# Kernel optimization log

Hardware: AMD Instinct MI355X
Metric: run time of the kernel (lower is better)

The kernel has to match this reference:

```python
import jax, jax.numpy as jnp
import numpy as np

N_NODES = 100000
N_EDGES = 1600000
N_GRAPHS = 2000
N_FEAT = 128
HIDDEN = 128
N_LAYERS = 4
BN_EPS = 1e-5


def setup_inputs() -> dict:
    key = jax.random.key(0)
    ks = jax.random.split(key, 8)
    x = jax.random.normal(ks[0], (N_NODES, N_FEAT), dtype=jnp.float32)
    edge_index = jax.random.randint(ks[1], (2, N_EDGES), 0, N_NODES, dtype=jnp.int32)
    batch = jnp.sort(jax.random.randint(ks[2], (N_NODES,), 0, N_GRAPHS, dtype=jnp.int32))
    # layer weights scaled down to keep activations stable over 4 layers
    Ws = jax.random.normal(ks[3], (N_LAYERS, HIDDEN, HIDDEN), dtype=jnp.float32) * 0.1
    bs = jnp.zeros((N_LAYERS, HIDDEN), jnp.float32)
    gammas = jnp.ones((N_LAYERS, HIDDEN), jnp.float32)
    betas = jnp.zeros((N_LAYERS, HIDDEN), jnp.float32)
    run_mean = jnp.zeros((N_LAYERS, HIDDEN), jnp.float32)
    run_var = jnp.ones((N_LAYERS, HIDDEN), jnp.float32)
    W_out = jax.random.normal(ks[4], (HIDDEN, 5), dtype=jnp.float32) * 0.1
    b_out = jnp.zeros((5,), jnp.float32)
    return {"x": x, "edge_index": edge_index, "batch": batch, "Ws": Ws, "bs": bs,
            "gammas": gammas, "betas": betas, "run_mean": run_mean, "run_var": run_var,
            "W_out": W_out, "b_out": b_out}


def _gcn_conv(x, src, dst, norm, self_coef, W, b):
    xw = x @ W                                        # [N, H]
    coef = norm[src] * norm[dst]                      # [E]
    msgs = xw[src] * coef[:, None]                    # [E, H] gather
    agg = jax.ops.segment_sum(msgs, dst, num_segments=N_NODES)  # scatter-add
    agg = agg + xw * self_coef[:, None]               # self-loop term
    return agg + b


def reference(x, edge_index, batch, Ws, bs, gammas, betas, run_mean, run_var, W_out, b_out):
    src, dst = edge_index[0], edge_index[1]
    # degree (incl. self-loop) from destination index
    deg = jax.ops.segment_sum(jnp.ones((N_EDGES,), x.dtype), dst, num_segments=N_NODES) + 1.0
    norm = jax.lax.rsqrt(deg)
    self_coef = norm * norm
    h = x
    for l in range(N_LAYERS):
        h = _gcn_conv(h, src, dst, norm, self_coef, Ws[l], bs[l])
        # BatchNorm1d in eval mode (running stats); dropout is identity in eval
        h = (h - run_mean[l]) * (gammas[l] * jax.lax.rsqrt(run_var[l] + BN_EPS)) + betas[l]
        h = jax.nn.relu(h)
    # global mean pool over graphs
    sums = jax.ops.segment_sum(h, batch, num_segments=N_GRAPHS)
    counts = jax.ops.segment_sum(jnp.ones((N_NODES,), h.dtype), batch, num_segments=N_GRAPHS)
    pooled = sums / jnp.maximum(counts, 1.0)[:, None]  # [G, H]
    return pooled @ W_out + b_out                      # [G, 5]
```

## Files before the change

kernel.cpp:

```cpp
#include <hip/hip_runtime.h>
#include <hip/hip_fp16.h>

#define N_NODES_C 100000
#define N_EDGES_C 1600000
#define N_GRAPHS_C 2000
#define HID 128
#define BN_EPS_C 1e-5f
#define NBUCK 391
#define PART_TILE 4096

typedef _Float16 half8 __attribute__((ext_vector_type(8)));
typedef float float4v __attribute__((ext_vector_type(4)));


__global__ __launch_bounds__(256) void kb_hist(const int* __restrict__ dst, int* __restrict__ bcount) {
    __shared__ int hist[NBUCK];
    const int t = threadIdx.x;
    for (int b = t; b < NBUCK; b += 256) hist[b] = 0;
    __syncthreads();
    const int e0 = blockIdx.x * PART_TILE;
    #pragma unroll
    for (int k = 0; k < 16; k++) {
        int e = e0 + k * 256 + t;
        if (e < N_EDGES_C) atomicAdd(&hist[dst[e] >> 8], 1);
    }
    __syncthreads();
    for (int b = t; b < NBUCK; b += 256) {
        int c = hist[b];
        if (c) atomicAdd(&bcount[b], c);
    }
}

__global__ __launch_bounds__(512) void kb_scan(const int* __restrict__ bcount,
                                               int* __restrict__ bbase, int* __restrict__ bcursor) {
    __shared__ int s[512];
    const int t = threadIdx.x;
    int v = (t < NBUCK) ? bcount[t] : 0;
    s[t] = v;
    __syncthreads();
    for (int off = 1; off < 512; off <<= 1) {
        int u = (t >= off) ? s[t - off] : 0;
        __syncthreads();
        s[t] += u;
        __syncthreads();
    }
    if (t < NBUCK) { int e = s[t] - v; bbase[t] = e; bcursor[t] = e; }
    if (t == 0) bbase[NBUCK] = N_EDGES_C;
}

__global__ __launch_bounds__(256) void kb_part(const int* __restrict__ src, const int* __restrict__ dst,
                                               int* __restrict__ bcursor, int* __restrict__ ebuf) {
    __shared__ int hist[NBUCK];
    __shared__ int startA[NBUCK];
    __shared__ int lcur[NBUCK];
    const int t = threadIdx.x;
    for (int b = t; b < NBUCK; b += 256) { hist[b] = 0; lcur[b] = 0; }
    __syncthreads();
    const int e0 = blockIdx.x * PART_TILE;
    #pragma unroll
    for (int k = 0; k < 16; k++) {
        int e = e0 + k * 256 + t;
        if (e < N_EDGES_C) atomicAdd(&hist[dst[e] >> 8], 1);
    }
    __syncthreads();
    for (int b = t; b < NBUCK; b += 256) {
        int c = hist[b];
        startA[b] = c ? atomicAdd(&bcursor[b], c) : 0;
    }
    __syncthreads();
    #pragma unroll
    for (int k = 0; k < 16; k++) {
        int e = e0 + k * 256 + t;
        if (e < N_EDGES_C) {
            int d = dst[e];
            int b = d >> 8;
            int pos = startA[b] + atomicAdd(&lcur[b], 1);
            ebuf[pos] = (src[e] << 8) | (d & 255);
        }
    }
}

__global__ __launch_bounds__(256) void kb_fill(const int* __restrict__ ebuf, const int* __restrict__ bbase,
                                               int* __restrict__ csr_src, int* __restrict__ offs,
                                               float* __restrict__ norm) {
    __shared__ int s[256];
    __shared__ int excl[256];
    __shared__ int lcur[256];
    const int b = blockIdx.x, t = threadIdx.x;
    const int base = b << 8;
    const int e0 = bbase[b], e1 = bbase[b + 1];
    s[t] = 0; lcur[t] = 0;
    __syncthreads();
    for (int e = e0 + t; e < e1; e += 256)
        atomicAdd(&s[ebuf[e] & 255], 1);
    __syncthreads();
    int own = s[t];
    for (int off = 1; off < 256; off <<= 1) {
        int v = (t >= off) ? s[t - off] : 0;
        __syncthreads();
        s[t] += v;
        __syncthreads();
    }
    excl[t] = s[t] - own;
    int node = base + t;
    if (node < N_NODES_C) {
        offs[node] = e0 + (s[t] - own);
        norm[node] = rsqrtf((float)own + 1.0f);
    }
    if (b == 0 && t == 0) offs[N_NODES_C] = N_EDGES_C;
    __syncthreads();
    for (int e = e0 + t; e < e1; e += 256) {
        int p = ebuf[e];
        int l = p & 255;
        int pos = e0 + excl[l] + atomicAdd(&lcur[l], 1);
        csr_src[pos] = p >> 8;
    }
}


__global__ __launch_bounds__(256) void k_tw(const float* __restrict__ Ws_all, _Float16* __restrict__ WT) {
    int idx = blockIdx.x * 256 + threadIdx.x;
    int l = idx >> 14, r = idx & 16383, k = r >> 7, n = r & 127;
    WT[l * 16384 + n * HID + k] = (_Float16)Ws_all[idx];
}


template<bool F32A>
__global__ __launch_bounds__(256) void k_gemm(const void* __restrict__ Ap,
                                              const _Float16* __restrict__ WT,
                                              const float* __restrict__ norm,
                                              _Float16* __restrict__ Y, int nrows) {
    __shared__ _Float16 Wt[HID][136];
    const int tid = threadIdx.x;
    #pragma unroll
    for (int t = 0; t < 8; t++) {
        int off = tid * 8 + t * 2048;
        half8 v = *(const half8*)&WT[off];
        *(half8*)&Wt[off >> 7][off & 127] = v;
    }
    __syncthreads();

    const int wave = tid >> 6, lane = tid & 63, quad = lane >> 4, l16 = lane & 15;
    half8 Wf[2][4];
    #pragma unroll
    for (int c = 0; c < 2; c++)
        #pragma unroll
        for (int ks = 0; ks < 4; ks++)
            Wf[c][ks] = *(const half8*)&Wt[(wave * 2 + c) * 16 + l16][ks * 32 + quad * 8];

    const int nbase = blockIdx.x * 128;
    #pragma unroll
    for (int t = 0; t < 8; t++) {
        int node = nbase + t * 16 + l16;
        bool ok = node < nrows;
        half8 Af[4];
        if (F32A) {
            const float* arow = (const float*)Ap + (long)node * HID;
            #pragma unroll
            for (int ks = 0; ks < 4; ks++) {
                if (ok) {
                    float4 fa = *(const float4*)&arow[ks * 32 + quad * 8];
                    float4 fb = *(const float4*)&arow[ks * 32 + quad * 8 + 4];
                    _Float16 pk[8] = {(_Float16)fa.x, (_Float16)fa.y, (_Float16)fa.z, (_Float16)fa.w,
                                      (_Float16)fb.x, (_Float16)fb.y, (_Float16)fb.z, (_Float16)fb.w};
                    Af[ks] = *(half8*)pk;
                } else Af[ks] = half8{};
            }
        } else {
            const _Float16* arow = (const _Float16*)Ap + (long)node * HID;
            #pragma unroll
            for (int ks = 0; ks < 4; ks++)
                Af[ks] = ok ? *(const half8*)&arow[ks * 32 + quad * 8] : half8{};
        }
        float4v a0 = {0.f, 0.f, 0.f, 0.f}, a1 = {0.f, 0.f, 0.f, 0.f};
        #pragma unroll
        for (int ks = 0; ks < 4; ks++) {
            a0 = __builtin_amdgcn_mfma_f32_16x16x32_f16(Wf[0][ks], Af[ks], a0, 0, 0, 0);
            a1 = __builtin_amdgcn_mfma_f32_16x16x32_f16(Wf[1][ks], Af[ks], a1, 0, 0, 0);
        }
        float nv = ok ? norm[node] : 0.f;
        _Float16 p0[4], p1[4];
        #pragma unroll
        for (int r = 0; r < 4; r++) {
            p0[r] = (_Float16)(a0[r] * nv);
            p1[r] = (_Float16)(a1[r] * nv);
        }
        *(ushort4*)&Y[(long)node * HID + (wave * 2 + 0) * 16 + quad * 4] = *(ushort4*)p0;
        *(ushort4*)&Y[(long)node * HID + (wave * 2 + 1) * 16 + quad * 4] = *(ushort4*)p1;
    }
}


__global__ __launch_bounds__(256) void k_agg(const __half* __restrict__ y, const int* __restrict__ offs,
                                             const int* __restrict__ csr_src, const float* __restrict__ norm,
                                             const float* __restrict__ bias, const float* __restrict__ mean,
                                             const float* __restrict__ gamma, const float* __restrict__ var,
                                             const float* __restrict__ beta, __half* __restrict__ h) {
    const int wave = __builtin_amdgcn_readfirstlane(threadIdx.x >> 6);
    const int lane = threadIdx.x & 63;
    const int i = blockIdx.x * 4 + wave;
    const int j = lane * 2;

    float2 f = __half22float2(*(const __half2*)&y[(long)i * HID + j]);
    float acc0 = f.x, acc1 = f.y;

    const int e0 = offs[i], e1 = offs[i + 1];
    int e = e0;
    do {
        int id[16];
        #pragma unroll
        for (int u = 0; u < 16; u++) {
            int raw = csr_src[e + u];
            id[u] = (e + u < e1) ? raw : N_NODES_C;
        }
        #pragma unroll
        for (int u = 0; u < 16; u++) {
            float2 g = __half22float2(*(const __half2*)&y[(long)id[u] * HID + j]);
            acc0 += g.x; acc1 += g.y;
        }
        e += 16;
    } while (e < e1);

    const float ni = norm[i];
    float2 bi = *(const float2*)&bias[j];
    float2 me = *(const float2*)&mean[j];
    float2 ga = *(const float2*)&gamma[j];
    float2 va = *(const float2*)&var[j];
    float2 be = *(const float2*)&beta[j];
    float v0 = (acc0 * ni + bi.x - me.x) * (ga.x * rsqrtf(va.x + BN_EPS_C)) + be.x;
    float v1 = (acc1 * ni + bi.y - me.y) * (ga.y * rsqrtf(va.y + BN_EPS_C)) + be.y;
    *(__half2*)&h[(long)i * HID + j] = __floats2half2_rn(fmaxf(v0, 0.f), fmaxf(v1, 0.f));
}


__global__ __launch_bounds__(128) void k_pool(const __half* __restrict__ h, const int* __restrict__ batch,
                                              float* __restrict__ psum, int* __restrict__ pcount) {
    const int j = threadIdx.x;
    const int i0 = blockIdx.x * 32;
    const int iend = min(i0 + 32, N_NODES_C);
    if (i0 >= N_NODES_C) return;
    float acc = 0.f;
    int cur = batch[i0];
    int runStart = i0;
    for (int i = i0; i < iend; i++) {
        int g = batch[i];
        if (g != cur) {
            atomicAdd(&psum[(long)cur * HID + j], acc);
            if (j == 0) atomicAdd(&pcount[cur], i - runStart);
            acc = 0.f; cur = g; runStart = i;
        }
        acc += __half2float(h[(long)i * HID + j]);
    }
    atomicAdd(&psum[(long)cur * HID + j], acc);
    if (j == 0) atomicAdd(&pcount[cur], iend - runStart);
}

__global__ __launch_bounds__(128) void k_final(const float* __restrict__ psum, const int* __restrict__ pcount,
                                               const float* __restrict__ W_out, const float* __restrict__ b_out,
                                               float* __restrict__ out) {
    __shared__ float red[128][5];
    const int g = blockIdx.x, j = threadIdx.x;
    float cnt = fmaxf((float)pcount[g], 1.f);
    float p = psum[(long)g * HID + j] / cnt;
    #pragma unroll
    for (int o = 0; o < 5; o++) red[j][o] = p * W_out[j * 5 + o];
    __syncthreads();
    for (int off = 64; off >= 1; off >>= 1) {
        if (j < off) {
            #pragma unroll
            for (int o = 0; o < 5; o++) red[j][o] += red[j + off][o];
        }
        __syncthreads();
    }
    if (j < 5) out[g * 5 + j] = red[0][j] + b_out[j];
}


extern "C" void kernel_launch(void* const* d_in, const int* in_sizes, int n_in,
                              void* d_out, int out_size, void* d_ws, size_t ws_size,
                              hipStream_t stream) {
    const float* x        = (const float*)d_in[0];
    const int*   eidx     = (const int*)d_in[1];
    const int*   src      = eidx;
    const int*   dst      = eidx + N_EDGES_C;
    const int*   batch    = (const int*)d_in[2];
    const float* Ws_all   = (const float*)d_in[3];
    const float* bs       = (const float*)d_in[4];
    const float* gammas   = (const float*)d_in[5];
    const float* betas    = (const float*)d_in[6];
    const float* run_mean = (const float*)d_in[7];
    const float* run_var  = (const float*)d_in[8];
    const float* W_out    = (const float*)d_in[9];
    const float* b_out    = (const float*)d_in[10];
    float* out = (float*)d_out;

    char* wp = (char*)d_ws;
    auto alloc = [&](size_t bytes) { char* p = wp; wp += (bytes + 255) & ~(size_t)255; return p; };
    __half*   h       = (__half*)alloc((size_t)N_NODES_C * HID * 2);
    _Float16* y       = (_Float16*)alloc((size_t)(N_NODES_C + 128) * HID * 2);
    int*      ebuf    = (int*)y;
    _Float16* WT      = (_Float16*)alloc((size_t)4 * HID * HID * 2);
    int*      csr_src = (int*)alloc((size_t)(N_EDGES_C + 16) * 4);
    int*      offs    = (int*)alloc((size_t)(N_NODES_C + 1) * 4);
    float*    norm    = (float*)alloc((size_t)N_NODES_C * 4);
    int*      bbase   = (int*)alloc((NBUCK + 1) * 4);
    int*      bcursor = (int*)alloc((NBUCK + 1) * 4);
    char*     zbeg    = wp;
    float*    psum    = (float*)alloc((size_t)N_GRAPHS_C * HID * 4);
    int*      pcount  = (int*)alloc((size_t)N_GRAPHS_C * 4);
    int*      bcount  = (int*)alloc((NBUCK + 1) * 4);
    size_t    zlen    = (size_t)(wp - zbeg);

    hipMemsetAsync(zbeg, 0, zlen, stream);

    k_tw<<<256, 256, 0, stream>>>(Ws_all, WT);

    const int PB = (N_EDGES_C + PART_TILE - 1) / PART_TILE;
    kb_hist<<<PB, 256, 0, stream>>>(dst, bcount);
    kb_scan<<<1, 512, 0, stream>>>(bcount, bbase, bcursor);
    kb_part<<<PB, 256, 0, stream>>>(src, dst, bcursor, ebuf);
    kb_fill<<<NBUCK, 256, 0, stream>>>(ebuf, bbase, csr_src, offs, norm);

    const int GB = (N_NODES_C + 127) / 128;
    const int AB = (N_NODES_C + 3) / 4;
    for (int l = 0; l < 4; l++) {
        const void* A = (l == 0) ? (const void*)x : (const void*)h;
        if (l == 0)
            k_gemm<true><<<GB, 256, 0, stream>>>(A, WT, norm, y, N_NODES_C);
        else
            k_gemm<false><<<GB, 256, 0, stream>>>(A, WT + (size_t)l * HID * HID, norm, y, N_NODES_C);
        k_agg<<<AB, 256, 0, stream>>>((const __half*)y, offs, csr_src, norm,
                                      bs + l * HID, run_mean + l * HID, gammas + l * HID,
                                      run_var + l * HID, betas + l * HID, (__half*)h);
    }
    const int PB2 = (N_NODES_C + 31) / 32;
    k_pool <<<PB2, 128, 0, stream>>>((const __half*)h, batch, psum, pcount);
    k_final<<<N_GRAPHS_C, 128, 0, stream>>>(psum, pcount, W_out, b_out, out);
}
```

Measured before the change: 502.0 us.

## Fuse all stages into one persistent cooperative kernel with grid syncs

Replaces the chain of separate launches (memset, weight transpose, CSR build, per-layer GEMM and aggregation, pooling, final projection) with a single cooperative persistent kernel. The stages are separated by grid.sync and use grid-stride loops over the old block indices. The intent is to remove per-launch overhead and inter-kernel gaps. In exchange it adds grid-wide barrier costs and limits the kernel to a fixed resident grid sized from occupancy, which may cut latency hiding in the gather-heavy aggregation phase.

Result: slower. 1.607 ms (+220.1%).

```diff
diff --git a/kernel.cpp b/kernel.cpp
--- a/kernel.cpp
+++ b/kernel.cpp
@@ -1,5 +1,8 @@
 #include <hip/hip_runtime.h>
 #include <hip/hip_fp16.h>
+#include <hip/hip_cooperative_groups.h>
+
+namespace cg = cooperative_groups;
 
 #define N_NODES_C 100000
 #define N_EDGES_C 1600000
@@ -8,271 +11,312 @@
 #define BN_EPS_C 1e-5f
 #define NBUCK 391
 #define PART_TILE 4096
+#define PB_C 391
+#define GB_C 782
+#define AB_C 25000
+#define PU_C 3125
 
 typedef _Float16 half8 __attribute__((ext_vector_type(8)));
 typedef float float4v __attribute__((ext_vector_type(4)));
 
-
-__global__ __launch_bounds__(256) void kb_hist(const int* __restrict__ dst, int* __restrict__ bcount) {
-    __shared__ int hist[NBUCK];
-    const int t = threadIdx.x;
-    for (int b = t; b < NBUCK; b += 256) hist[b] = 0;
-    __syncthreads();
-    const int e0 = blockIdx.x * PART_TILE;
-    #pragma unroll
-    for (int k = 0; k < 16; k++) {
-        int e = e0 + k * 256 + t;
-        if (e < N_EDGES_C) atomicAdd(&hist[dst[e] >> 8], 1);
-    }
-    __syncthreads();
-    for (int b = t; b < NBUCK; b += 256) {
-        int c = hist[b];
-        if (c) atomicAdd(&bcount[b], c);
-    }
-}
-
-__global__ __launch_bounds__(512) void kb_scan(const int* __restrict__ bcount,
-                                               int* __restrict__ bbase, int* __restrict__ bcursor) {
-    __shared__ int s[512];
-    const int t = threadIdx.x;
-    int v = (t < NBUCK) ? bcount[t] : 0;
-    s[t] = v;
-    __syncthreads();
-    for (int off = 1; off < 512; off <<= 1) {
-        int u = (t >= off) ? s[t - off] : 0;
-        __syncthreads();
-        s[t] += u;
-        __syncthreads();
-    }
-    if (t < NBUCK) { int e = s[t] - v; bbase[t] = e; bcursor[t] = e; }
-    if (t == 0) bbase[NBUCK] = N_EDGES_C;
-}
-
-__global__ __launch_bounds__(256) void kb_part(const int* __restrict__ src, const int* __restrict__ dst,
-                                               int* __restrict__ bcursor, int* __restrict__ ebuf) {
-    __shared__ int hist[NBUCK];
-    __shared__ int startA[NBUCK];
-    __shared__ int lcur[NBUCK];
-    const int t = threadIdx.x;
-    for (int b = t; b < NBUCK; b += 256) { hist[b] = 0; lcur[b] = 0; }
-    __syncthreads();
-    const int e0 = blockIdx.x * PART_TILE;
-    #pragma unroll
-    for (int k = 0; k < 16; k++) {
-        int e = e0 + k * 256 + t;
-        if (e < N_EDGES_C) atomicAdd(&hist[dst[e] >> 8], 1);
-    }
-    __syncthreads();
-    for (int b = t; b < NBUCK; b += 256) {
-        int c = hist[b];
-        startA[b] = c ? atomicAdd(&bcursor[b], c) : 0;
-    }
-    __syncthreads();
-    #pragma unroll
-    for (int k = 0; k < 16; k++) {
-        int e = e0 + k * 256 + t;
-        if (e < N_EDGES_C) {
-            int d = dst[e];
-            int b = d >> 8;
-            int pos = startA[b] + atomicAdd(&lcur[b], 1);
-            ebuf[pos] = (src[e] << 8) | (d & 255);
-        }
-    }
-}
-
-__global__ __launch_bounds__(256) void kb_fill(const int* __restrict__ ebuf, const int* __restrict__ bbase,
-                                               int* __restrict__ csr_src, int* __restrict__ offs,
-                                               float* __restrict__ norm) {
-    __shared__ int s[256];
-    __shared__ int excl[256];
-    __shared__ int lcur[256];
-    const int b = blockIdx.x, t = threadIdx.x;
-    const int base = b << 8;
-    const int e0 = bbase[b], e1 = bbase[b + 1];
-    s[t] = 0; lcur[t] = 0;
-    __syncthreads();
-    for (int e = e0 + t; e < e1; e += 256)
-        atomicAdd(&s[ebuf[e] & 255], 1);
-    __syncthreads();
-    int own = s[t];
-    for (int off = 1; off < 256; off <<= 1) {
-        int v = (t >= off) ? s[t - off] : 0;
-        __syncthreads();
-        s[t] += v;
-        __syncthreads();
-    }
-    excl[t] = s[t] - own;
-    int node = base + t;
-    if (node < N_NODES_C) {
-        offs[node] = e0 + (s[t] - own);
-        norm[node] = rsqrtf((float)own + 1.0f);
-    }
-    if (b == 0 && t == 0) offs[N_NODES_C] = N_EDGES_C;
-    __syncthreads();
-    for (int e = e0 + t; e < e1; e += 256) {
-        int p = ebuf[e];
-        int l = p & 255;
-        int pos = e0 + excl[l] + atomicAdd(&lcur[l], 1);
-        csr_src[pos] = p >> 8;
-    }
-}
-
-
-__global__ __launch_bounds__(256) void k_tw(const float* __restrict__ Ws_all, _Float16* __restrict__ WT) {
-    int idx = blockIdx.x * 256 + threadIdx.x;
-    int l = idx >> 14, r = idx & 16383, k = r >> 7, n = r & 127;
-    WT[l * 16384 + n * HID + k] = (_Float16)Ws_all[idx];
-}
-
-
-template<bool F32A>
-__global__ __launch_bounds__(256) void k_gemm(const void* __restrict__ Ap,
-                                              const _Float16* __restrict__ WT,
-                                              const float* __restrict__ norm,
-                                              _Float16* __restrict__ Y, int nrows) {
-    __shared__ _Float16 Wt[HID][136];
-    const int tid = threadIdx.x;
-    #pragma unroll
-    for (int t = 0; t < 8; t++) {
-        int off = tid * 8 + t * 2048;
-        half8 v = *(const half8*)&WT[off];
-        *(half8*)&Wt[off >> 7][off & 127] = v;
-    }
-    __syncthreads();
-
-    const int wave = tid >> 6, lane = tid & 63, quad = lane >> 4, l16 = lane & 15;
-    half8 Wf[2][4];
-    #pragma unroll
-    for (int c = 0; c < 2; c++)
-        #pragma unroll
-        for (int ks = 0; ks < 4; ks++)
-            Wf[c][ks] = *(const half8*)&Wt[(wave * 2 + c) * 16 + l16][ks * 32 + quad * 8];
-
-    const int nbase = blockIdx.x * 128;
-    #pragma unroll
-    for (int t = 0; t < 8; t++) {
-        int node = nbase + t * 16 + l16;
-        bool ok = node < nrows;
-        half8 Af[4];
-        if (F32A) {
-            const float* arow = (const float*)Ap + (long)node * HID;
-            #pragma unroll
-            for (int ks = 0; ks < 4; ks++) {
-                if (ok) {
-                    float4 fa = *(const float4*)&arow[ks * 32 + quad * 8];
-                    float4 fb = *(const float4*)&arow[ks * 32 + quad * 8 + 4];
-                    _Float16 pk[8] = {(_Float16)fa.x, (_Float16)fa.y, (_Float16)fa.z, (_Float16)fa.w,
-                                      (_Float16)fb.x, (_Float16)fb.y, (_Float16)fb.z, (_Float16)fb.w};
-                    Af[ks] = *(half8*)pk;
-                } else Af[ks] = half8{};
+constexpr size_t al(size_t v) { return (v + 255) & ~(size_t)255; }
+constexpr size_t OFF_H    = 0;
+constexpr size_t OFF_Y    = al(OFF_H    + (size_t)N_NODES_C * HID * 2);
+constexpr size_t OFF_WT   = al(OFF_Y    + (size_t)(N_NODES_C + 128) * HID * 2);
+constexpr size_t OFF_CSR  = al(OFF_WT   + (size_t)4 * HID * HID * 2);
+constexpr size_t OFF_OFFS = al(OFF_CSR  + (size_t)(N_EDGES_C + 16) * 4);
+constexpr size_t OFF_NORM = al(OFF_OFFS + (size_t)(N_NODES_C + 1) * 4);
+constexpr size_t OFF_BB   = al(OFF_NORM + (size_t)N_NODES_C * 4);
+constexpr size_t OFF_BCUR = al(OFF_BB   + (NBUCK + 1) * 4);
+constexpr size_t OFF_ZERO = al(OFF_BCUR + (NBUCK + 1) * 4);
+constexpr size_t OFF_PSUM = OFF_ZERO;
+constexpr size_t OFF_PCNT = al(OFF_PSUM + (size_t)N_GRAPHS_C * HID * 4);
+constexpr size_t OFF_BCNT = al(OFF_PCNT + (size_t)N_GRAPHS_C * 4);
+constexpr size_t OFF_END  = al(OFF_BCNT + (NBUCK + 1) * 4);
+
+union SM {
+    _Float16 Wt[HID][136];
+    struct { int hist[NBUCK], startA[NBUCK], lcur[NBUCK]; } part;
+    struct { int s[256], excl[256], lcur[256]; } fill;
+    int scan[512];
+    float red[2][128][5];
+};
+
+__global__ __launch_bounds__(256, 4) void k_mega(
+    const float* __restrict__ x, const int* __restrict__ eidx, const int* __restrict__ batch,
+    const float* __restrict__ Ws_all, const float* __restrict__ bs, const float* __restrict__ gammas,
+    const float* __restrict__ betas, const float* __restrict__ run_mean, const float* __restrict__ run_var,
+    const float* __restrict__ W_out, const float* __restrict__ b_out, float* __restrict__ out,
+    char* __restrict__ ws)
+{
+    __shared__ SM sm;
+    cg::grid_group grid = cg::this_grid();
+    const int tid = threadIdx.x, bid = blockIdx.x, G = gridDim.x;
+    const int* src = eidx;
+    const int* dst = eidx + N_EDGES_C;
+
+    __half*   h      = (__half*)(ws + OFF_H);
+    _Float16* y      = (_Float16*)(ws + OFF_Y);
+    int*      ebuf   = (int*)(ws + OFF_Y);
+    _Float16* WT     = (_Float16*)(ws + OFF_WT);
+    int*      csr    = (int*)(ws + OFF_CSR);
+    int*      offs   = (int*)(ws + OFF_OFFS);
+    float*    norm   = (float*)(ws + OFF_NORM);
+    int*      bbase  = (int*)(ws + OFF_BB);
+    int*      bcur   = (int*)(ws + OFF_BCUR);
+    float*    psum   = (float*)(ws + OFF_PSUM);
+    int*      pcount = (int*)(ws + OFF_PCNT);
+    int*      bcount = (int*)(ws + OFF_BCNT);
+
+    {
+        int* zp = (int*)(ws + OFF_ZERO);
+        const int zn = (int)((OFF_END - OFF_ZERO) >> 2);
+        for (int i = bid * 256 + tid; i < zn; i += G * 256) zp[i] = 0;
+        for (int i = bid * 256 + tid; i < 4 * HID * HID; i += G * 256) {
+            int l = i >> 14, r = i & 16383, k = r >> 7, n = r & 127;
+            WT[l * 16384 + n * HID + k] = (_Float16)Ws_all[i];
+        }
+    }
+    grid.sync();
+
+    for (int c = bid; c < PB_C; c += G) {
+        for (int b = tid; b < NBUCK; b += 256) sm.part.hist[b] = 0;
+        __syncthreads();
+        const int e0 = c * PART_TILE;
+        #pragma unroll
+        for (int k = 0; k < 16; k++) {
+            int e = e0 + k * 256 + tid;
+            if (e < N_EDGES_C) atomicAdd(&sm.part.hist[dst[e] >> 8], 1);
+        }
+        __syncthreads();
+        for (int b = tid; b < NBUCK; b += 256) {
+            int cc = sm.part.hist[b];
+            if (cc) atomicAdd(&bcount[b], cc);
+        }
+        __syncthreads();
+    }
+    grid.sync();
+
+    if (bid == 0) {
+        int v0 = (tid < NBUCK) ? bcount[tid] : 0;
+        int v1 = (tid + 256 < NBUCK) ? bcount[tid + 256] : 0;
+        sm.scan[tid] = v0; sm.scan[tid + 256] = v1;
+        __syncthreads();
+        for (int off = 1; off < 512; off <<= 1) {
+            int a = (tid >= off) ? sm.scan[tid - off] : 0;
+            int b = (tid + 256 >= off) ? sm.scan[tid + 256 - off] : 0;
+            __syncthreads();
+            sm.scan[tid] += a; sm.scan[tid + 256] += b;
+            __syncthreads();
+        }
+        if (tid < NBUCK) { int e = sm.scan[tid] - v0; bbase[tid] = e; bcur[tid] = e; }
+        if (tid + 256 < NBUCK) { int e = sm.scan[tid + 256] - v1; bbase[tid + 256] = e; bcur[tid + 256] = e; }
+        if (tid == 0) bbase[NBUCK] = N_EDGES_C;
+    }
+    grid.sync();
+
+    for (int c = bid; c < PB_C; c += G) {
+        for (int b = tid; b < NBUCK; b += 256) { sm.part.hist[b] = 0; sm.part.lcur[b] = 0; }
+        __syncthreads();
+        const int e0 = c * PART_TILE;
+        #pragma unroll
+        for (int k = 0; k < 16; k++) {
+            int e = e0 + k * 256 + tid;
+            if (e < N_EDGES_C) atomicAdd(&sm.part.hist[dst[e] >> 8], 1);
+        }
+        __syncthreads();
+        for (int b = tid; b < NBUCK; b += 256) {
+            int cc = sm.part.hist[b];
+            sm.part.startA[b] = cc ? atomicAdd(&bcur[b], cc) : 0;
+        }
+        __syncthreads();
+        #pragma unroll
+        for (int k = 0; k < 16; k++) {
+            int e = e0 + k * 256 + tid;
+            if (e < N_EDGES_C) {
+                int d = dst[e];
+                int b = d >> 8;
+                int pos = sm.part.startA[b] + atomicAdd(&sm.part.lcur[b], 1);
+                ebuf[pos] = (src[e] << 8) | (d & 255);
             }
-        } else {
-            const _Float16* arow = (const _Float16*)Ap + (long)node * HID;
+        }
+        __syncthreads();
+    }
+    grid.sync();
+
+    for (int b = bid; b < NBUCK; b += G) {
+        const int base = b << 8;
+        const int e0 = bbase[b], e1 = bbase[b + 1];
+        sm.fill.s[tid] = 0; sm.fill.lcur[tid] = 0;
+        __syncthreads();
+        for (int e = e0 + tid; e < e1; e += 256)
+            atomicAdd(&sm.fill.s[ebuf[e] & 255], 1);
+        __syncthreads();
+        int own = sm.fill.s[tid];
+        for (int off = 1; off < 256; off <<= 1) {
+            int v = (tid >= off) ? sm.fill.s[tid - off] : 0;
+            __syncthreads();
+            sm.fill.s[tid] += v;
+            __syncthreads();
+        }
+        sm.fill.excl[tid] = sm.fill.s[tid] - own;
+        int node = base + tid;
+        if (node < N_NODES_C) {
+            offs[node] = e0 + sm.fill.excl[tid];
+            norm[node] = rsqrtf((float)own + 1.0f);
+        }
+        if (b == 0 && tid == 0) offs[N_NODES_C] = N_EDGES_C;
+        __syncthreads();
+        for (int e = e0 + tid; e < e1; e += 256) {
+            int p = ebuf[e];
+            int l = p & 255;
+            int pos = e0 + sm.fill.excl[l] + atomicAdd(&sm.fill.lcur[l], 1);
+            csr[pos] = p >> 8;
+        }
+        __syncthreads();
+    }
+    grid.sync();
+
+    const int wv = __builtin_amdgcn_readfirstlane(tid >> 6);
+    const int lane = tid & 63, quad = lane >> 4, l16 = lane & 15;
+    const int j = lane * 2;
+    const __half* yh = (const __half*)y;
+
+    for (int l = 0; l < 4; ++l) {
+        const _Float16* WTl = WT + (size_t)l * 16384;
+        #pragma unroll
+        for (int t = 0; t < 8; t++) {
+            int off = tid * 8 + t * 2048;
+            *(half8*)&sm.Wt[off >> 7][off & 127] = *(const half8*)&WTl[off];
+        }
+        __syncthreads();
+        half8 Wf[2][4];
+        #pragma unroll
+        for (int c = 0; c < 2; c++)
             #pragma unroll
             for (int ks = 0; ks < 4; ks++)
-                Af[ks] = ok ? *(const half8*)&arow[ks * 32 + quad * 8] : half8{};
-        }
-        float4v a0 = {0.f, 0.f, 0.f, 0.f}, a1 = {0.f, 0.f, 0.f, 0.f};
-        #pragma unroll
-        for (int ks = 0; ks < 4; ks++) {
-            a0 = __builtin_amdgcn_mfma_f32_16x16x32_f16(Wf[0][ks], Af[ks], a0, 0, 0, 0);
-            a1 = __builtin_amdgcn_mfma_f32_16x16x32_f16(Wf[1][ks], Af[ks], a1, 0, 0, 0);
-        }
-        float nv = ok ? norm[node] : 0.f;
-        _Float16 p0[4], p1[4];
-        #pragma unroll
-        for (int r = 0; r < 4; r++) {
-            p0[r] = (_Float16)(a0[r] * nv);
-            p1[r] = (_Float16)(a1[r] * nv);
-        }
-        *(ushort4*)&Y[(long)node * HID + (wave * 2 + 0) * 16 + quad * 4] = *(ushort4*)p0;
-        *(ushort4*)&Y[(long)node * HID + (wave * 2 + 1) * 16 + quad * 4] = *(ushort4*)p1;
-    }
-}
-
-
-__global__ __launch_bounds__(256) void k_agg(const __half* __restrict__ y, const int* __restrict__ offs,
-                                             const int* __restrict__ csr_src, const float* __restrict__ norm,
-                                             const float* __restrict__ bias, const float* __restrict__ mean,
-                                             const float* __restrict__ gamma, const float* __restrict__ var,
-                                             const float* __restrict__ beta, __half* __restrict__ h) {
-    const int wave = __builtin_amdgcn_readfirstlane(threadIdx.x >> 6);
-    const int lane = threadIdx.x & 63;
-    const int i = blockIdx.x * 4 + wave;
-    const int j = lane * 2;
-
-    float2 f = __half22float2(*(const __half2*)&y[(long)i * HID + j]);
-    float acc0 = f.x, acc1 = f.y;
-
-    const int e0 = offs[i], e1 = offs[i + 1];
-    int e = e0;
-    do {
-        int id[16];
-        #pragma unroll
-        for (int u = 0; u < 16; u++) {
-            int raw = csr_src[e + u];
-            id[u] = (e + u < e1) ? raw : N_NODES_C;
-        }
-        #pragma unroll
-        for (int u = 0; u < 16; u++) {
-            float2 g = __half22float2(*(const __half2*)&y[(long)id[u] * HID + j]);
-            acc0 += g.x; acc1 += g.y;
-        }
-        e += 16;
-    } while (e < e1);
-
-    const float ni = norm[i];
-    float2 bi = *(const float2*)&bias[j];
-    float2 me = *(const float2*)&mean[j];
-    float2 ga = *(const float2*)&gamma[j];
-    float2 va = *(const float2*)&var[j];
-    float2 be = *(const float2*)&beta[j];
-    float v0 = (acc0 * ni + bi.x - me.x) * (ga.x * rsqrtf(va.x + BN_EPS_C)) + be.x;
-    float v1 = (acc1 * ni + bi.y - me.y) * (ga.y * rsqrtf(va.y + BN_EPS_C)) + be.y;
-    *(__half2*)&h[(long)i * HID + j] = __floats2half2_rn(fmaxf(v0, 0.f), fmaxf(v1, 0.f));
-}
-
-
-__global__ __launch_bounds__(128) void k_pool(const __half* __restrict__ h, const int* __restrict__ batch,
-                                              float* __restrict__ psum, int* __restrict__ pcount) {
-    const int j = threadIdx.x;
-    const int i0 = blockIdx.x * 32;
-    const int iend = min(i0 + 32, N_NODES_C);
-    if (i0 >= N_NODES_C) return;
-    float acc = 0.f;
-    int cur = batch[i0];
-    int runStart = i0;
-    for (int i = i0; i < iend; i++) {
-        int g = batch[i];
-        if (g != cur) {
-            atomicAdd(&psum[(long)cur * HID + j], acc);
-            if (j == 0) atomicAdd(&pcount[cur], i - runStart);
-            acc = 0.f; cur = g; runStart = i;
-        }
-        acc += __half2float(h[(long)i * HID + j]);
-    }
-    atomicAdd(&psum[(long)cur * HID + j], acc);
-    if (j == 0) atomicAdd(&pcount[cur], iend - runStart);
-}
-
-__global__ __launch_bounds__(128) void k_final(const float* __restrict__ psum, const int* __restrict__ pcount,
-                                               const float* __restrict__ W_out, const float* __restrict__ b_out,
-                                               float* __restrict__ out) {
-    __shared__ float red[128][5];
-    const int g = blockIdx.x, j = threadIdx.x;
-    float cnt = fmaxf((float)pcount[g], 1.f);
-    float p = psum[(long)g * HID + j] / cnt;
-    #pragma unroll
-    for (int o = 0; o < 5; o++) red[j][o] = p * W_out[j * 5 + o];
-    __syncthreads();
-    for (int off = 64; off >= 1; off >>= 1) {
-        if (j < off) {
+                Wf[c][ks] = *(const half8*)&sm.Wt[(wv * 2 + c) * 16 + l16][ks * 32 + quad * 8];
+
+        for (int tile = bid; tile < GB_C; tile += G) {
+            const int nbase = tile * 128;
             #pragma unroll
-            for (int o = 0; o < 5; o++) red[j][o] += red[j + off][o];
-        }
-        __syncthreads();
-    }
-    if (j < 5) out[g * 5 + j] = red[0][j] + b_out[j];
+            for (int t = 0; t < 8; t++) {
+                int node = nbase + t * 16 + l16;
+                bool ok = node < N_NODES_C;
+                half8 Af[4];
+                if (l == 0) {
+                    const float* arow = x + (long)node * HID;
+                    #pragma unroll
+                    for (int ks = 0; ks < 4; ks++) {
+                        if (ok) {
+                            float4 fa = *(const float4*)&arow[ks * 32 + quad * 8];
+                            float4 fb = *(const float4*)&arow[ks * 32 + quad * 8 + 4];
+                            _Float16 pk[8] = {(_Float16)fa.x, (_Float16)fa.y, (_Float16)fa.z, (_Float16)fa.w,
+                                              (_Float16)fb.x, (_Float16)fb.y, (_Float16)fb.z, (_Float16)fb.w};
+                            Af[ks] = *(half8*)pk;
+                        } else Af[ks] = half8{};
+                    }
+                } else {
+                    const _Float16* arow = (const _Float16*)h + (long)node * HID;
+                    #pragma unroll
+                    for (int ks = 0; ks < 4; ks++)
+                        Af[ks] = ok ? *(const half8*)&arow[ks * 32 + quad * 8] : half8{};
+                }
+                float4v a0 = {0.f, 0.f, 0.f, 0.f}, a1 = {0.f, 0.f, 0.f, 0.f};
+                #pragma unroll
+                for (int ks = 0; ks < 4; ks++) {
+                    a0 = __builtin_amdgcn_mfma_f32_16x16x32_f16(Wf[0][ks], Af[ks], a0, 0, 0, 0);
+                    a1 = __builtin_amdgcn_mfma_f32_16x16x32_f16(Wf[1][ks], Af[ks], a1, 0, 0, 0);
+                }
+                float nv = ok ? norm[node] : 0.f;
+                _Float16 p0[4], p1[4];
+                #pragma unroll
+                for (int r = 0; r < 4; r++) {
+                    p0[r] = (_Float16)(a0[r] * nv);
+                    p1[r] = (_Float16)(a1[r] * nv);
+                }
+                *(ushort4*)&y[(long)node * HID + (wv * 2 + 0) * 16 + quad * 4] = *(ushort4*)p0;
+                *(ushort4*)&y[(long)node * HID + (wv * 2 + 1) * 16 + quad * 4] = *(ushort4*)p1;
+            }
+        }
+        grid.sync();
+
+        const float* bias = bs + l * HID;
+        const float* mean = run_mean + l * HID;
+        const float* gam  = gammas + l * HID;
+        const float* varr = run_var + l * HID;
+        const float* bet  = betas + l * HID;
+        for (int grp = bid; grp < AB_C; grp += G) {
+            const int i = grp * 4 + wv;
+            float2 f = __half22float2(*(const __half2*)&yh[(long)i * HID + j]);
+            float acc0 = f.x, acc1 = f.y;
+            const int e0 = offs[i], e1 = offs[i + 1];
+            int e = e0;
+            do {
+                int id[16];
+                #pragma unroll
+                for (int u = 0; u < 16; u++) {
+                    int raw = csr[e + u];
+                    id[u] = (e + u < e1) ? raw : N_NODES_C;
+                }
+                #pragma unroll
+                for (int u = 0; u < 16; u++) {
+                    float2 g2 = __half22float2(*(const __half2*)&yh[(long)id[u] * HID + j]);
+                    acc0 += g2.x; acc1 += g2.y;
+                }
+                e += 16;
+            } while (e < e1);
+            const float ni = norm[i];
+            float2 bi = *(const float2*)&bias[j];
+            float2 me = *(const float2*)&mean[j];
+            float2 ga = *(const float2*)&gam[j];
+            float2 va = *(const float2*)&varr[j];
+            float2 be = *(const float2*)&bet[j];
+            float v0 = (acc0 * ni + bi.x - me.x) * (ga.x * rsqrtf(va.x + BN_EPS_C)) + be.x;
+            float v1 = (acc1 * ni + bi.y - me.y) * (ga.y * rsqrtf(va.y + BN_EPS_C)) + be.y;
+            *(__half2*)&h[(long)i * HID + j] = __floats2half2_rn(fmaxf(v0, 0.f), fmaxf(v1, 0.f));
+        }
+        grid.sync();
+    }
+
+    const int sub = tid >> 7, t7 = tid & 127;
+    for (int u = 2 * bid + sub; u < PU_C; u += 2 * G) {
+        const int i0 = u * 32;
+        const int iend = min(i0 + 32, N_NODES_C);
+        float acc = 0.f;
+        int cur = batch[i0];
+        int runStart = i0;
+        for (int i = i0; i < iend; i++) {
+            int g = batch[i];
+            if (g != cur) {
+                atomicAdd(&psum[(long)cur * HID + t7], acc);
+                if (t7 == 0) atomicAdd(&pcount[cur], i - runStart);
+                acc = 0.f; cur = g; runStart = i;
+            }
+            acc += __half2float(h[(long)i * HID + t7]);
+        }
+        atomicAdd(&psum[(long)cur * HID + t7], acc);
+        if (t7 == 0) atomicAdd(&pcount[cur], iend - runStart);
+    }
+    grid.sync();
+
+    for (int base = 2 * bid; base < N_GRAPHS_C; base += 2 * G) {
+        const int g = base + sub;
+        float cnt = fmaxf((float)pcount[g], 1.f);
+        float p = psum[(long)g * HID + t7] / cnt;
+        #pragma unroll
+        for (int o = 0; o < 5; o++) sm.red[sub][t7][o] = p * W_out[t7 * 5 + o];
+        __syncthreads();
+        for (int off = 64; off >= 1; off >>= 1) {
+            if (t7 < off) {
+                #pragma unroll
+                for (int o = 0; o < 5; o++) sm.red[sub][t7][o] += sm.red[sub][t7 + off][o];
+            }
+            __syncthreads();
+        }
+        if (t7 < 5) out[g * 5 + t7] = sm.red[sub][0][t7] + b_out[t7];
+        __syncthreads();
+    }
 }
 
 
@@ -281,8 +325,6 @@
                               hipStream_t stream) {
     const float* x        = (const float*)d_in[0];
     const int*   eidx     = (const int*)d_in[1];
-    const int*   src      = eidx;
-    const int*   dst      = eidx + N_EDGES_C;
     const int*   batch    = (const int*)d_in[2];
     const float* Ws_all   = (const float*)d_in[3];
     const float* bs       = (const float*)d_in[4];
@@ -293,47 +335,15 @@
     const float* W_out    = (const float*)d_in[9];
     const float* b_out    = (const float*)d_in[10];
     float* out = (float*)d_out;
-
-    char* wp = (char*)d_ws;
-    auto alloc = [&](size_t bytes) { char* p = wp; wp += (bytes + 255) & ~(size_t)255; return p; };
-    __half*   h       = (__half*)alloc((size_t)N_NODES_C * HID * 2);
-    _Float16* y       = (_Float16*)alloc((size_t)(N_NODES_C + 128) * HID * 2);
-    int*      ebuf    = (int*)y;
-    _Float16* WT      = (_Float16*)alloc((size_t)4 * HID * HID * 2);
-    int*      csr_src = (int*)alloc((size_t)(N_EDGES_C + 16) * 4);
-    int*      offs    = (int*)alloc((size_t)(N_NODES_C + 1) * 4);
-    float*    norm    = (float*)alloc((size_t)N_NODES_C * 4);
-    int*      bbase   = (int*)alloc((NBUCK + 1) * 4);
-    int*      bcursor = (int*)alloc((NBUCK + 1) * 4);
-    char*     zbeg    = wp;
-    float*    psum    = (float*)alloc((size_t)N_GRAPHS_C * HID * 4);
-    int*      pcount  = (int*)alloc((size_t)N_GRAPHS_C * 4);
-    int*      bcount  = (int*)alloc((NBUCK + 1) * 4);
-    size_t    zlen    = (size_t)(wp - zbeg);
-
-    hipMemsetAsync(zbeg, 0, zlen, stream);
-
-    k_tw<<<256, 256, 0, stream>>>(Ws_all, WT);
-
-    const int PB = (N_EDGES_C + PART_TILE - 1) / PART_TILE;
-    kb_hist<<<PB, 256, 0, stream>>>(dst, bcount);
-    kb_scan<<<1, 512, 0, stream>>>(bcount, bbase, bcursor);
-    kb_part<<<PB, 256, 0, stream>>>(src, dst, bcursor, ebuf);
-    kb_fill<<<NBUCK, 256, 0, stream>>>(ebuf, bbase, csr_src, offs, norm);
-
-    const int GB = (N_NODES_C + 127) / 128;
-    const int AB = (N_NODES_C + 3) / 4;
-    for (int l = 0; l < 4; l++) {
-        const void* A = (l == 0) ? (const void*)x : (const void*)h;
-        if (l == 0)
-            k_gemm<true><<<GB, 256, 0, stream>>>(A, WT, norm, y, N_NODES_C);
-        else
-            k_gemm<false><<<GB, 256, 0, stream>>>(A, WT + (size_t)l * HID * HID, norm, y, N_NODES_C);
-        k_agg<<<AB, 256, 0, stream>>>((const __half*)y, offs, csr_src, norm,
-                                      bs + l * HID, run_mean + l * HID, gammas + l * HID,
-                                      run_var + l * HID, betas + l * HID, (__half*)h);
-    }
-    const int PB2 = (N_NODES_C + 31) / 32;
-    k_pool <<<PB2, 128, 0, stream>>>((const __half*)h, batch, psum, pcount);
-    k_final<<<N_GRAPHS_C, 128, 0, stream>>>(psum, pcount, W_out, b_out, out);
+    char* ws = (char*)d_ws;
+
+    int nb = 0;
+    if (hipOccupancyMaxActiveBlocksPerMultiprocessor(&nb, k_mega, 256, 0) != hipSuccess || nb < 1) nb = 2;
+    if (nb > 8) nb = 8;
+    unsigned grid = (unsigned)nb * 256u;
+
+    void* args[] = {(void*)&x, (void*)&eidx, (void*)&batch, (void*)&Ws_all, (void*)&bs,
+                    (void*)&gammas, (void*)&betas, (void*)&run_mean, (void*)&run_var,
+                    (void*)&W_out, (void*)&b_out, (void*)&out, (void*)&ws};
+    hipLaunchCooperativeKernel(k_mega, dim3(grid), dim3(256), args, 0, stream);
 }
```

## Fuse aggregation, BN/ReLU and next-layer GEMM into one kernel per layer

Applied to the files above, without the earlier changes.

Each layer's aggregation and BN/ReLU now writes its 32-node output tile to shared memory, and the same block multiplies that tile by the next layer's weights with MFMA. This removes the h round-trip through global memory and the separate GEMM launches. The last layer does mean-pooling directly from shared memory, and the weight transpose is merged into the histogram kernel to save launches. The change adds ping-pong y buffers and zeroes a padding row of yB, which gathers of the sentinel index read. The fused kernel runs 512 threads per block, and weights are loaded straight from global memory by each block.

Result: faster. 458.8 us (-8.6%).

```diff
diff --git a/kernel.cpp b/kernel.cpp
--- a/kernel.cpp
+++ b/kernel.cpp
@@ -13,9 +13,17 @@
 typedef float float4v __attribute__((ext_vector_type(4)));
 
 
-__global__ __launch_bounds__(256) void kb_hist(const int* __restrict__ dst, int* __restrict__ bcount) {
+__global__ __launch_bounds__(256) void k_twhist(const float* __restrict__ Ws_all, _Float16* __restrict__ WT,
+                                                const int* __restrict__ dst, int* __restrict__ bcount,
+                                                _Float16* __restrict__ yB_dummy) {
+    const int t = threadIdx.x;
+    int idx = blockIdx.x * 256 + t;
+    if (idx < 4 * HID * HID) {
+        int l = idx >> 14, r = idx & 16383, k = r >> 7, n = r & 127;
+        WT[l * 16384 + n * HID + k] = (_Float16)Ws_all[idx];
+    }
+    if (blockIdx.x == 390 && t < 64) ((int*)yB_dummy)[t] = 0;
     __shared__ int hist[NBUCK];
-    const int t = threadIdx.x;
     for (int b = t; b < NBUCK; b += 256) hist[b] = 0;
     __syncthreads();
     const int e0 = blockIdx.x * PART_TILE;
@@ -118,25 +126,16 @@
 }
 
 
-__global__ __launch_bounds__(256) void k_tw(const float* __restrict__ Ws_all, _Float16* __restrict__ WT) {
-    int idx = blockIdx.x * 256 + threadIdx.x;
-    int l = idx >> 14, r = idx & 16383, k = r >> 7, n = r & 127;
-    WT[l * 16384 + n * HID + k] = (_Float16)Ws_all[idx];
-}
-
-
-template<bool F32A>
-__global__ __launch_bounds__(256) void k_gemm(const void* __restrict__ Ap,
-                                              const _Float16* __restrict__ WT,
-                                              const float* __restrict__ norm,
-                                              _Float16* __restrict__ Y, int nrows) {
+__global__ __launch_bounds__(256) void k_gemm0(const float* __restrict__ Ap,
+                                               const _Float16* __restrict__ WT,
+                                               const float* __restrict__ norm,
+                                               _Float16* __restrict__ Y, int nrows) {
     __shared__ _Float16 Wt[HID][136];
     const int tid = threadIdx.x;
     #pragma unroll
     for (int t = 0; t < 8; t++) {
         int off = tid * 8 + t * 2048;
-        half8 v = *(const half8*)&WT[off];
-        *(half8*)&Wt[off >> 7][off & 127] = v;
+        *(half8*)&Wt[off >> 7][off & 127] = *(const half8*)&WT[off];
     }
     __syncthreads();
 
@@ -154,23 +153,16 @@
         int node = nbase + t * 16 + l16;
         bool ok = node < nrows;
         half8 Af[4];
-        if (F32A) {
-            const float* arow = (const float*)Ap + (long)node * HID;
-            #pragma unroll
-            for (int ks = 0; ks < 4; ks++) {
-                if (ok) {
-                    float4 fa = *(const float4*)&arow[ks * 32 + quad * 8];
-                    float4 fb = *(const float4*)&arow[ks * 32 + quad * 8 + 4];
-                    _Float16 pk[8] = {(_Float16)fa.x, (_Float16)fa.y, (_Float16)fa.z, (_Float16)fa.w,
-                                      (_Float16)fb.x, (_Float16)fb.y, (_Float16)fb.z, (_Float16)fb.w};
-                    Af[ks] = *(half8*)pk;
-                } else Af[ks] = half8{};
-            }
-        } else {
-            const _Float16* arow = (const _Float16*)Ap + (long)node * HID;
-            #pragma unroll
-            for (int ks = 0; ks < 4; ks++)
-                Af[ks] = ok ? *(const half8*)&arow[ks * 32 + quad * 8] : half8{};
+        const float* arow = Ap + (long)node * HID;
+        #pragma unroll
+        for (int ks = 0; ks < 4; ks++) {
+            if (ok) {
+                float4 fa = *(const float4*)&arow[ks * 32 + quad * 8];
+                float4 fb = *(const float4*)&arow[ks * 32 + quad * 8 + 4];
+                _Float16 pk[8] = {(_Float16)fa.x, (_Float16)fa.y, (_Float16)fa.z, (_Float16)fa.w,
+                                  (_Float16)fb.x, (_Float16)fb.y, (_Float16)fb.z, (_Float16)fb.w};
+                Af[ks] = *(half8*)pk;
+            } else Af[ks] = half8{};
         }
         float4v a0 = {0.f, 0.f, 0.f, 0.f}, a1 = {0.f, 0.f, 0.f, 0.f};
         #pragma unroll
@@ -191,68 +183,97 @@
 }
 
 
-__global__ __launch_bounds__(256) void k_agg(const __half* __restrict__ y, const int* __restrict__ offs,
-                                             const int* __restrict__ csr_src, const float* __restrict__ norm,
-                                             const float* __restrict__ bias, const float* __restrict__ mean,
-                                             const float* __restrict__ gamma, const float* __restrict__ var,
-                                             const float* __restrict__ beta, __half* __restrict__ h) {
-    const int wave = __builtin_amdgcn_readfirstlane(threadIdx.x >> 6);
-    const int lane = threadIdx.x & 63;
-    const int i = blockIdx.x * 4 + wave;
+template<bool LAST>
+__global__ __launch_bounds__(512, 8) void k_fused(
+    const __half* __restrict__ yin, _Float16* __restrict__ yout,
+    const _Float16* __restrict__ WTn, const int* __restrict__ offs,
+    const int* __restrict__ csr, const float* __restrict__ norm,
+    const float* __restrict__ bias, const float* __restrict__ mean,
+    const float* __restrict__ gam, const float* __restrict__ varr,
+    const float* __restrict__ bet, const int* __restrict__ batch,
+    float* __restrict__ psum, int* __restrict__ pcount)
+{
+    __shared__ __half ht[32][136];
+    const int tid = threadIdx.x;
+    const int wv = __builtin_amdgcn_readfirstlane(tid >> 6);
+    const int lane = tid & 63;
     const int j = lane * 2;
-
-    float2 f = __half22float2(*(const __half2*)&y[(long)i * HID + j]);
-    float acc0 = f.x, acc1 = f.y;
-
-    const int e0 = offs[i], e1 = offs[i + 1];
-    int e = e0;
-    do {
-        int id[16];
-        #pragma unroll
-        for (int u = 0; u < 16; u++) {
-            int raw = csr_src[e + u];
-            id[u] = (e + u < e1) ? raw : N_NODES_C;
-        }
-        #pragma unroll
-        for (int u = 0; u < 16; u++) {
-            float2 g = __half22float2(*(const __half2*)&y[(long)id[u] * HID + j]);
-            acc0 += g.x; acc1 += g.y;
-        }
-        e += 16;
-    } while (e < e1);
-
-    const float ni = norm[i];
-    float2 bi = *(const float2*)&bias[j];
-    float2 me = *(const float2*)&mean[j];
-    float2 ga = *(const float2*)&gamma[j];
-    float2 va = *(const float2*)&var[j];
-    float2 be = *(const float2*)&beta[j];
-    float v0 = (acc0 * ni + bi.x - me.x) * (ga.x * rsqrtf(va.x + BN_EPS_C)) + be.x;
-    float v1 = (acc1 * ni + bi.y - me.y) * (ga.y * rsqrtf(va.y + BN_EPS_C)) + be.y;
-    *(__half2*)&h[(long)i * HID + j] = __floats2half2_rn(fmaxf(v0, 0.f), fmaxf(v1, 0.f));
-}
-
-
-__global__ __launch_bounds__(128) void k_pool(const __half* __restrict__ h, const int* __restrict__ batch,
-                                              float* __restrict__ psum, int* __restrict__ pcount) {
-    const int j = threadIdx.x;
-    const int i0 = blockIdx.x * 32;
-    const int iend = min(i0 + 32, N_NODES_C);
-    if (i0 >= N_NODES_C) return;
-    float acc = 0.f;
-    int cur = batch[i0];
-    int runStart = i0;
-    for (int i = i0; i < iend; i++) {
-        int g = batch[i];
-        if (g != cur) {
-            atomicAdd(&psum[(long)cur * HID + j], acc);
-            if (j == 0) atomicAdd(&pcount[cur], i - runStart);
-            acc = 0.f; cur = g; runStart = i;
-        }
-        acc += __half2float(h[(long)i * HID + j]);
-    }
-    atomicAdd(&psum[(long)cur * HID + j], acc);
-    if (j == 0) atomicAdd(&pcount[cur], iend - runStart);
+    const int nbase = blockIdx.x * 32;
+
+    for (int r = 0; r < 4; r++) {
+        const int li = wv * 4 + r;
+        const int i = nbase + li;
+        float2 f = __half22float2(*(const __half2*)&yin[(long)i * HID + j]);
+        float acc0 = f.x, acc1 = f.y;
+        const int e0 = offs[i], e1 = offs[i + 1];
+        int e = e0;
+        do {
+            int id[16];
+            #pragma unroll
+            for (int u = 0; u < 16; u++) {
+                int raw = csr[e + u];
+                id[u] = (e + u < e1) ? raw : N_NODES_C;
+            }
+            #pragma unroll
+            for (int u = 0; u < 16; u++) {
+                float2 g2 = __half22float2(*(const __half2*)&yin[(long)id[u] * HID + j]);
+                acc0 += g2.x; acc1 += g2.y;
+            }
+            e += 16;
+        } while (e < e1);
+        const float ni = norm[i];
+        float2 bi = *(const float2*)&bias[j];
+        float2 me = *(const float2*)&mean[j];
+        float2 ga = *(const float2*)&gam[j];
+        float2 va = *(const float2*)&varr[j];
+        float2 be = *(const float2*)&bet[j];
+        float v0 = (acc0 * ni + bi.x - me.x) * (ga.x * rsqrtf(va.x + BN_EPS_C)) + be.x;
+        float v1 = (acc1 * ni + bi.y - me.y) * (ga.y * rsqrtf(va.y + BN_EPS_C)) + be.y;
+        *(__half2*)&ht[li][j] = __floats2half2_rn(fmaxf(v0, 0.f), fmaxf(v1, 0.f));
+    }
+    __syncthreads();
+
+    if constexpr (!LAST) {
+        const int quad = lane >> 4, l16 = lane & 15;
+        half8 Wf[4];
+        #pragma unroll
+        for (int ks = 0; ks < 4; ks++)
+            Wf[ks] = *(const half8*)&WTn[(long)(wv * 16 + l16) * HID + ks * 32 + quad * 8];
+        #pragma unroll
+        for (int ng = 0; ng < 2; ng++) {
+            half8 Af[4];
+            #pragma unroll
+            for (int ks = 0; ks < 4; ks++)
+                Af[ks] = *(const half8*)&ht[ng * 16 + l16][ks * 32 + quad * 8];
+            float4v a0 = {0.f, 0.f, 0.f, 0.f};
+            #pragma unroll
+            for (int ks = 0; ks < 4; ks++)
+                a0 = __builtin_amdgcn_mfma_f32_16x16x32_f16(Wf[ks], Af[ks], a0, 0, 0, 0);
+            const int node = nbase + ng * 16 + l16;
+            const float nv = norm[node];
+            _Float16 p[4];
+            #pragma unroll
+            for (int r = 0; r < 4; r++) p[r] = (_Float16)(a0[r] * nv);
+            *(ushort4*)&yout[(long)node * HID + wv * 16 + quad * 4] = *(ushort4*)p;
+        }
+    } else {
+        const int sub = tid >> 7, t7 = tid & 127;
+        const int i0 = nbase + sub * 8, iend = i0 + 8;
+        float acc = 0.f;
+        int cur = batch[i0];
+        int runStart = i0;
+        for (int i = i0; i < iend; i++) {
+            int g = batch[i];
+            if (g != cur) {
+                atomicAdd(&psum[(long)cur * HID + t7], acc);
+                if (t7 == 0) atomicAdd(&pcount[cur], i - runStart);
+                acc = 0.f; cur = g; runStart = i;
+            }
+            acc += __half2float(ht[i - nbase][t7]);
+        }
+        atomicAdd(&psum[(long)cur * HID + t7], acc);
+        if (t7 == 0) atomicAdd(&pcount[cur], iend - runStart);
+    }
 }
 
 __global__ __launch_bounds__(128) void k_final(const float* __restrict__ psum, const int* __restrict__ pcount,
@@ -296,9 +317,9 @@
 
     char* wp = (char*)d_ws;
     auto alloc = [&](size_t bytes) { char* p = wp; wp += (bytes + 255) & ~(size_t)255; return p; };
-    __half*   h       = (__half*)alloc((size_t)N_NODES_C * HID * 2);
-    _Float16* y       = (_Float16*)alloc((size_t)(N_NODES_C + 128) * HID * 2);
-    int*      ebuf    = (int*)y;
+    _Float16* yA      = (_Float16*)alloc((size_t)(N_NODES_C + 128) * HID * 2);
+    _Float16* yB      = (_Float16*)alloc((size_t)(N_NODES_C + 128) * HID * 2);
+    int*      ebuf    = (int*)yA;
     _Float16* WT      = (_Float16*)alloc((size_t)4 * HID * HID * 2);
     int*      csr_src = (int*)alloc((size_t)(N_EDGES_C + 16) * 4);
     int*      offs    = (int*)alloc((size_t)(N_NODES_C + 1) * 4);
@@ -313,27 +334,28 @@
 
     hipMemsetAsync(zbeg, 0, zlen, stream);
 
-    k_tw<<<256, 256, 0, stream>>>(Ws_all, WT);
-
     const int PB = (N_EDGES_C + PART_TILE - 1) / PART_TILE;
-    kb_hist<<<PB, 256, 0, stream>>>(dst, bcount);
-    kb_scan<<<1, 512, 0, stream>>>(bcount, bbase, bcursor);
-    kb_part<<<PB, 256, 0, stream>>>(src, dst, bcursor, ebuf);
-    kb_fill<<<NBUCK, 256, 0, stream>>>(ebuf, bbase, csr_src, offs, norm);
+    k_twhist<<<PB, 256, 0, stream>>>(Ws_all, WT, dst, bcount, yB + (size_t)N_NODES_C * HID);
+    kb_scan <<<1, 512, 0, stream>>>(bcount, bbase, bcursor);
+    kb_part <<<PB, 256, 0, stream>>>(src, dst, bcursor, ebuf);
+    kb_fill <<<NBUCK, 256, 0, stream>>>(ebuf, bbase, csr_src, offs, norm);
 
     const int GB = (N_NODES_C + 127) / 128;
-    const int AB = (N_NODES_C + 3) / 4;
-    for (int l = 0; l < 4; l++) {
-        const void* A = (l == 0) ? (const void*)x : (const void*)h;
-        if (l == 0)
-            k_gemm<true><<<GB, 256, 0, stream>>>(A, WT, norm, y, N_NODES_C);
-        else
-            k_gemm<false><<<GB, 256, 0, stream>>>(A, WT + (size_t)l * HID * HID, norm, y, N_NODES_C);
-        k_agg<<<AB, 256, 0, stream>>>((const __half*)y, offs, csr_src, norm,
-                                      bs + l * HID, run_mean + l * HID, gammas + l * HID,
-                                      run_var + l * HID, betas + l * HID, (__half*)h);
-    }
-    const int PB2 = (N_NODES_C + 31) / 32;
-    k_pool <<<PB2, 128, 0, stream>>>((const __half*)h, batch, psum, pcount);
+    const int FB = N_NODES_C / 32;
+    k_gemm0<<<GB, 256, 0, stream>>>(x, WT, norm, yA, N_NODES_C);
+
+    k_fused<false><<<FB, 512, 0, stream>>>((const __half*)yA, yB, WT + 1 * 16384, offs, csr_src, norm,
+                                           bs + 0 * HID, run_mean + 0 * HID, gammas + 0 * HID,
+                                           run_var + 0 * HID, betas + 0 * HID, nullptr, nullptr, nullptr);
+    k_fused<false><<<FB, 512, 0, stream>>>((const __half*)yB, yA, WT + 2 * 16384, offs, csr_src, norm,
+                                           bs + 1 * HID, run_mean + 1 * HID, gammas + 1 * HID,
+                                           run_var + 1 * HID, betas + 1 * HID, nullptr, nullptr, nullptr);
+    k_fused<false><<<FB, 512, 0, stream>>>((const __half*)yA, yB, WT + 3 * 16384, offs, csr_src, norm,
+                                           bs + 2 * HID, run_mean + 2 * HID, gammas + 2 * HID,
+                                           run_var + 2 * HID, betas + 2 * HID, nullptr, nullptr, nullptr);
+    k_fused<true><<<FB, 512, 0, stream>>>((const __half*)yB, nullptr, nullptr, offs, csr_src, norm,
+                                          bs + 3 * HID, run_mean + 3 * HID, gammas + 3 * HID,
+                                          run_var + 3 * HID, betas + 3 * HID, batch, psum, pcount);
+
     k_final<<<N_GRAPHS_C, 128, 0, stream>>>(psum, pcount, W_out, b_out, out);
 }
```
